# Optimization experiments

Hardware: AMD Instinct MI355X
Metric: run time of the kernel (lower is better)

Reference implementation:

```python
import jax, jax.numpy as jnp
import numpy as np


def setup_inputs() -> dict:
    key = jax.random.key(0)
    ks = jax.random.split(key, 9)
    U, H, R, N = 32, 5120, 160, 16
    return {
        "x": jax.random.normal(ks[0], (U, H), jnp.float32),
        "W_delta": jax.random.normal(ks[1], (H, R), jnp.float32) * 0.02,
        "W_dt": jax.random.normal(ks[2], (R, H), jnp.float32) * 0.02,
        "b_dt": jax.random.normal(ks[3], (H,), jnp.float32) * 0.02,
        "W_B": jax.random.normal(ks[4], (H, N), jnp.float32) * 0.02,
        "W_C": jax.random.normal(ks[5], (H, N), jnp.float32) * 0.02,
        "A_log": jax.random.uniform(ks[6], (H, N), jnp.float32),
        "D": jax.random.normal(ks[7], (H,), jnp.float32),
        "h": jax.random.normal(ks[8], (U, H, N), jnp.float32),
    }


def reference(x, W_delta, W_dt, b_dt, W_B, W_C, A_log, D, h):
    # x: (U,H) single-token decode for U users; h: (U,H,N) recurrent state.
    # delta: low-rank projection then dt_proj, softplus
    dt = jax.nn.softplus((x @ W_delta) @ W_dt + b_dt)          # (U,H)
    A = -jnp.exp(A_log)                                        # (H,N)
    abar = jnp.exp(dt[:, :, None] * A[None, :, :])             # (U,H,N)
    B = x @ W_B                                                # (U,N)
    C = x @ W_C                                                # (U,N)
    # state update: h' = abar*h + (dt*B)*x
    h_new = abar * h + dt[:, :, None] * B[:, None, :] * x[:, :, None]  # (U,H,N)
    # output mix: y = C . h' + D*x
    y = jnp.einsum("uhn,un->uh", h_new, C) + x * D[None, :]    # (U,H)
    return y
```

## Files before the change

kernel.cpp:

```cpp
#include <hip/hip_runtime.h>
#include <math.h>

#define UU 32
#define HH 5120
#define RR 160
#define NN 16


__device__ __forceinline__ unsigned short f2bf(float f) {
    unsigned int u = __float_as_uint(f);
    u += 0x7fffu + ((u >> 16) & 1u);
    return (unsigned short)(u >> 16);
}
__device__ __forceinline__ float blo(unsigned int v) { return __uint_as_float(v << 16); }
__device__ __forceinline__ float bhi(unsigned int v) { return __uint_as_float(v & 0xffff0000u); }

__global__ __launch_bounds__(256) void proj_kernel(
    const float* __restrict__ x, const float* __restrict__ Wd,
    const float* __restrict__ WB, const float* __restrict__ WC,
    float* __restrict__ ws)
{
    __shared__ float xs[32 * 36];
    __shared__ float wt[32 * 160];

    const int b = blockIdx.x;
    const int t = threadIdx.x;

    if (b < 80) {
        const int u0 = (t >> 5) * 4;
        const int r0 = (t & 31) * 5;
        float acc[4][5];
        #pragma unroll
        for (int i = 0; i < 4; i++)
            #pragma unroll
            for (int j = 0; j < 5; j++) acc[i][j] = 0.f;

        #pragma unroll
        for (int c = 0; c < 2; c++) {
            const int k0 = b * 64 + c * 32;
            if (c) __syncthreads();
            #pragma unroll
            for (int i = 0; i < 4; i++) {
                int idx = t + i * 256;
                int u = idx >> 5, kk = idx & 31;
                xs[kk * 36 + u] = x[u * HH + k0 + kk];
            }
            #pragma unroll
            for (int i = 0; i < 5; i++) {
                int idx4 = t + i * 256;
                *(float4*)&wt[idx4 * 4] = ((const float4*)(Wd + k0 * RR))[idx4];
            }
            __syncthreads();

            #pragma unroll
            for (int kk = 0; kk < 32; kk++) {
                float4 xv = *(const float4*)&xs[kk * 36 + u0];
                float wv[5];
                #pragma unroll
                for (int j = 0; j < 5; j++) wv[j] = wt[kk * 160 + r0 + j];
                const float xi[4] = {xv.x, xv.y, xv.z, xv.w};
                #pragma unroll
                for (int i = 0; i < 4; i++)
                    #pragma unroll
                    for (int j = 0; j < 5; j++) acc[i][j] += xi[i] * wv[j];
            }
        }
        #pragma unroll
        for (int i = 0; i < 4; i++)
            #pragma unroll
            for (int j = 0; j < 5; j++)
                atomicAdd(&ws[(u0 + i) * 160 + (r0 + j)], acc[i][j]);
    } else {
        const int bc = b - 80;
        const int k0 = bc * 160;
        const int n = t & 15;
        const int uu = t >> 4;
        const float* xa = x + uu * HH;
        const float* xb = x + (uu + 16) * HH;
        float aB0 = 0.f, aB1 = 0.f, aC0 = 0.f, aC1 = 0.f;
        #pragma unroll 8
        for (int k = k0; k < k0 + 160; k++) {
            float wb = WB[k * NN + n];
            float wc = WC[k * NN + n];
            float va = xa[k], vb = xb[k];
            aB0 += va * wb; aB1 += vb * wb;
            aC0 += va * wc; aC1 += vb * wc;
        }
        atomicAdd(&ws[5120 + uu * 16 + n], aB0);
        atomicAdd(&ws[5120 + (uu + 16) * 16 + n], aB1);
        atomicAdd(&ws[5632 + uu * 16 + n], aC0);
        atomicAdd(&ws[5632 + (uu + 16) * 16 + n], aC1);
    }
}

__device__ __forceinline__ float softplusf(float v) {
    return (v > 20.f) ? v : log1pf(expf(v));
}

__global__ __launch_bounds__(256) void ssm_kernel(
    const float* __restrict__ x, const float* __restrict__ Wdt,
    const float* __restrict__ bdt, const float* __restrict__ Alog,
    const float* __restrict__ Dv, const float* __restrict__ hstate,
    const float* __restrict__ ws, float* __restrict__ y)
{
    __shared__ unsigned short tmp_b[32 * 168];
    __shared__ unsigned short wsl_b[16 * 168];
    __shared__ float Bl[32 * 20];
    __shared__ float Cl[32 * 20];
    __shared__ float an_l[16 * 20];
    __shared__ float xl[32 * 17];
    __shared__ float bdtl[16];
    __shared__ float Dl[16];

    const int t  = threadIdx.x;
    const int h0 = blockIdx.x * 16;
    const int u  = t >> 3;
    const int q  = t & 7;

    const float* hb0 = hstate + (size_t)(u * HH + h0 + q) * 16;
    const float* hb1 = hstate + (size_t)(u * HH + h0 + q + 8) * 16;
    float4 hv0[4], hv1[4];
    #pragma unroll
    for (int k = 0; k < 4; k++) { hv0[k] = ((const float4*)hb0)[k]; hv1[k] = ((const float4*)hb1)[k]; }

    #pragma unroll
    for (int i = 0; i < 5; i++) {
        int idx4 = t + i * 256;
        int uu = idx4 / 40, r4 = idx4 % 40;
        float4 v = ((const float4*)ws)[idx4];
        unsigned int p0 = (unsigned int)f2bf(v.x) | ((unsigned int)f2bf(v.y) << 16);
        unsigned int p1 = (unsigned int)f2bf(v.z) | ((unsigned int)f2bf(v.w) << 16);
        *(uint2*)&tmp_b[uu * 168 + r4 * 4] = make_uint2(p0, p1);
    }
    #pragma unroll
    for (int i = 0; i < 10; i++) {
        int idx = t + i * 256;
        int r = idx >> 4, hh = idx & 15;
        wsl_b[hh * 168 + r] = f2bf(Wdt[r * HH + h0 + hh]);
    }
    #pragma unroll
    for (int i = 0; i < 2; i++) {
        int idx = t + i * 256;
        int uu = idx >> 4, n = idx & 15;
        Bl[uu * 20 + n] = ws[5120 + idx];
        Cl[uu * 20 + n] = ws[5632 + idx];
        xl[uu * 17 + n] = x[uu * HH + h0 + n];
    }
    {
        int hh = t >> 4, n = t & 15;
        an_l[hh * 20 + n] = -expf(Alog[(h0 + hh) * 16 + n]);
    }
    if (t < 16) { bdtl[t] = bdt[h0 + t]; Dl[t] = Dv[h0 + t]; }
    __syncthreads();

    const uint4* ta = (const uint4*)&tmp_b[u * 168];
    const uint4* w0p = (const uint4*)&wsl_b[q * 168];
    const uint4* w1p = (const uint4*)&wsl_b[(q + 8) * 168];
    float a0e = 0.f, a0o = 0.f, a1e = 0.f, a1o = 0.f;
    #pragma unroll
    for (int c = 0; c < 20; c++) {
        uint4 av = ta[c];
        uint4 w0 = w0p[c];
        uint4 w1 = w1p[c];
        #define MAC(X) \
            a0e += blo(av.X) * blo(w0.X); a0o += bhi(av.X) * bhi(w0.X); \
            a1e += blo(av.X) * blo(w1.X); a1o += bhi(av.X) * bhi(w1.X);
        MAC(x) MAC(y) MAC(z) MAC(w)
        #undef MAC
    }
    const float dt0 = softplusf(bdtl[q]     + (a0e + a0o));
    const float dt1 = softplusf(bdtl[q + 8] + (a1e + a1o));

    #pragma unroll
    for (int j = 0; j < 2; j++) {
        const int hh = q + j * 8;
        const float dt = j ? dt1 : dt0;
        const float xv = xl[u * 17 + hh];
        const float K  = dt * xv;
        float yv = xv * Dl[hh];
        const float4* hv = j ? hv1 : hv0;
        #pragma unroll
        for (int qq = 0; qq < 4; qq++) {
            float4 h4 = hv[qq];
            float4 bq = *(const float4*)&Bl[u * 20 + qq * 4];
            float4 cq = *(const float4*)&Cl[u * 20 + qq * 4];
            float4 av = *(const float4*)&an_l[hh * 20 + qq * 4];
            yv += (expf(dt * av.x) * h4.x + K * bq.x) * cq.x;
            yv += (expf(dt * av.y) * h4.y + K * bq.y) * cq.y;
            yv += (expf(dt * av.z) * h4.z + K * bq.z) * cq.z;
            yv += (expf(dt * av.w) * h4.w + K * bq.w) * cq.w;
        }
        y[u * HH + h0 + hh] = yv;
    }
}

extern "C" void kernel_launch(void* const* d_in, const int* in_sizes, int n_in,
                              void* d_out, int out_size, void* d_ws, size_t ws_size,
                              hipStream_t stream) {
    const float* x    = (const float*)d_in[0];
    const float* Wd   = (const float*)d_in[1];
    const float* Wdt  = (const float*)d_in[2];
    const float* bdt  = (const float*)d_in[3];
    const float* WB   = (const float*)d_in[4];
    const float* WC   = (const float*)d_in[5];
    const float* Alog = (const float*)d_in[6];
    const float* Dv   = (const float*)d_in[7];
    const float* hst  = (const float*)d_in[8];
    float* y  = (float*)d_out;
    float* ws = (float*)d_ws;

    proj_kernel<<<112, 256, 0, stream>>>(x, Wd, WB, WC, ws);
    ssm_kernel<<<320, 256, 0, stream>>>(x, Wdt, bdt, Alog, Dv, hst, ws, y);
}
```

Before: 113.8 us.

## Replace atomic accumulation with split-K partial buffers reduced in consumer kernel

The projection kernel now writes per-split partial sums of the low-rank delta and B/C projections into separate workspace slices instead of using atomicAdd on shared locations. The SSM kernel sums the 16 slices while staging data into shared memory. The SSM kernel also moves to 512 threads with one channel per thread. This removes atomic contention and any need for a zeroed workspace, at the cost of every SSM block redundantly re-reading and reducing the partial buffers.

```diff
diff --git a/kernel.cpp b/kernel.cpp
--- a/kernel.cpp
+++ b/kernel.cpp
@@ -6,6 +6,10 @@
 #define RR 160
 #define NN 16
 
+
+#define TMP_WS 0
+#define BP_WS  81920
+#define CP_WS  90112
 
 __device__ __forceinline__ unsigned short f2bf(float f) {
     unsigned int u = __float_as_uint(f);
@@ -21,23 +25,21 @@
     float* __restrict__ ws)
 {
     __shared__ float xs[32 * 36];
-    __shared__ float wt[32 * 160];
+    __shared__ float wt[32 * 32];
 
     const int b = blockIdx.x;
     const int t = threadIdx.x;
 
     if (b < 80) {
+        const int s  = b & 15;
+        const int rt = b >> 4;
+        const int r0 = rt * 32;
         const int u0 = (t >> 5) * 4;
-        const int r0 = (t & 31) * 5;
-        float acc[4][5];
-        #pragma unroll
-        for (int i = 0; i < 4; i++)
-            #pragma unroll
-            for (int j = 0; j < 5; j++) acc[i][j] = 0.f;
-
-        #pragma unroll
-        for (int c = 0; c < 2; c++) {
-            const int k0 = b * 64 + c * 32;
+        const int r  = t & 31;
+        float acc[4] = {0.f, 0.f, 0.f, 0.f};
+
+        for (int c = 0; c < 10; c++) {
+            const int k0 = s * 320 + c * 32;
             if (c) __syncthreads();
             #pragma unroll
             for (int i = 0; i < 4; i++) {
@@ -45,51 +47,49 @@
                 int u = idx >> 5, kk = idx & 31;
                 xs[kk * 36 + u] = x[u * HH + k0 + kk];
             }
-            #pragma unroll
-            for (int i = 0; i < 5; i++) {
-                int idx4 = t + i * 256;
-                *(float4*)&wt[idx4 * 4] = ((const float4*)(Wd + k0 * RR))[idx4];
+            {
+                int kk = t >> 3, c4 = t & 7;
+                *(float4*)&wt[kk * 32 + c4 * 4] =
+                    *(const float4*)(Wd + (size_t)(k0 + kk) * RR + r0 + c4 * 4);
             }
             __syncthreads();
 
             #pragma unroll
             for (int kk = 0; kk < 32; kk++) {
                 float4 xv = *(const float4*)&xs[kk * 36 + u0];
-                float wv[5];
-                #pragma unroll
-                for (int j = 0; j < 5; j++) wv[j] = wt[kk * 160 + r0 + j];
-                const float xi[4] = {xv.x, xv.y, xv.z, xv.w};
-                #pragma unroll
-                for (int i = 0; i < 4; i++)
-                    #pragma unroll
-                    for (int j = 0; j < 5; j++) acc[i][j] += xi[i] * wv[j];
+                float wv = wt[kk * 32 + r];
+                acc[0] += xv.x * wv; acc[1] += xv.y * wv;
+                acc[2] += xv.z * wv; acc[3] += xv.w * wv;
             }
         }
         #pragma unroll
         for (int i = 0; i < 4; i++)
-            #pragma unroll
-            for (int j = 0; j < 5; j++)
-                atomicAdd(&ws[(u0 + i) * 160 + (r0 + j)], acc[i][j]);
+            ws[TMP_WS + s * 5120 + (u0 + i) * 160 + r0 + r] = acc[i];
     } else {
-        const int bc = b - 80;
-        const int k0 = bc * 160;
-        const int n = t & 15;
+        const int sb = b - 80;
+        const int k0 = sb * 320;
+        const int n  = t & 15;
         const int uu = t >> 4;
-        const float* xa = x + uu * HH;
-        const float* xb = x + (uu + 16) * HH;
+        const float* xa = x + uu * HH + k0;
+        const float* xb = x + (uu + 16) * HH + k0;
         float aB0 = 0.f, aB1 = 0.f, aC0 = 0.f, aC1 = 0.f;
-        #pragma unroll 8
-        for (int k = k0; k < k0 + 160; k++) {
-            float wb = WB[k * NN + n];
-            float wc = WC[k * NN + n];
-            float va = xa[k], vb = xb[k];
-            aB0 += va * wb; aB1 += vb * wb;
-            aC0 += va * wc; aC1 += vb * wc;
-        }
-        atomicAdd(&ws[5120 + uu * 16 + n], aB0);
-        atomicAdd(&ws[5120 + (uu + 16) * 16 + n], aB1);
-        atomicAdd(&ws[5632 + uu * 16 + n], aC0);
-        atomicAdd(&ws[5632 + (uu + 16) * 16 + n], aC1);
+        #pragma unroll 2
+        for (int k4 = 0; k4 < 80; k4++) {
+            float4 va = *(const float4*)(xa + k4 * 4);
+            float4 vb = *(const float4*)(xb + k4 * 4);
+            const int kb = (k0 + k4 * 4) * NN + n;
+            #define STEP(D, CMP) { \
+                float wb = WB[kb + (D) * NN]; \
+                float wc = WC[kb + (D) * NN]; \
+                aB0 += va.CMP * wb; aB1 += vb.CMP * wb; \
+                aC0 += va.CMP * wc; aC1 += vb.CMP * wc; }
+            STEP(0, x) STEP(1, y) STEP(2, z) STEP(3, w)
+            #undef STEP
+        }
+        ws[BP_WS + sb * 512 + uu * 16 + n]        = aB0;
+        ws[BP_WS + sb * 512 + (uu + 16) * 16 + n] = aB1;
+        ws[CP_WS + sb * 512 + uu * 16 + n]        = aC0;
+        ws[CP_WS + sb * 512 + (uu + 16) * 16 + n] = aC1;
     }
 }
 
@@ -97,7 +97,7 @@
     return (v > 20.f) ? v : log1pf(expf(v));
 }
 
-__global__ __launch_bounds__(256) void ssm_kernel(
+__global__ __launch_bounds__(512) void ssm_kernel(
     const float* __restrict__ x, const float* __restrict__ Wdt,
     const float* __restrict__ bdt, const float* __restrict__ Alog,
     const float* __restrict__ Dv, const float* __restrict__ hstate,
@@ -114,39 +114,49 @@
 
     const int t  = threadIdx.x;
     const int h0 = blockIdx.x * 16;
-    const int u  = t >> 3;
-    const int q  = t & 7;
-
-    const float* hb0 = hstate + (size_t)(u * HH + h0 + q) * 16;
-    const float* hb1 = hstate + (size_t)(u * HH + h0 + q + 8) * 16;
-    float4 hv0[4], hv1[4];
-    #pragma unroll
-    for (int k = 0; k < 4; k++) { hv0[k] = ((const float4*)hb0)[k]; hv1[k] = ((const float4*)hb1)[k]; }
-
+    const int u  = t >> 4;
+    const int q  = t & 15;
+
+    const float* hb = hstate + (size_t)(u * HH + h0 + q) * 16;
+    float4 hv[4];
+    #pragma unroll
+    for (int k = 0; k < 4; k++) hv[k] = ((const float4*)hb)[k];
+
+    #pragma unroll
+    for (int i = 0; i < 3; i++) {
+        int idx4 = t + i * 512;
+        if (idx4 < 1280) {
+            float sx = 0.f, sy = 0.f, sz = 0.f, sw = 0.f;
+            #pragma unroll
+            for (int s = 0; s < 16; s++) {
+                float4 v = ((const float4*)(ws + TMP_WS + s * 5120))[idx4];
+                sx += v.x; sy += v.y; sz += v.z; sw += v.w;
+            }
+            int uu = idx4 / 40, r4 = idx4 % 40;
+            unsigned int p0 = (unsigned int)f2bf(sx) | ((unsigned int)f2bf(sy) << 16);
+            unsigned int p1 = (unsigned int)f2bf(sz) | ((unsigned int)f2bf(sw) << 16);
+            *(uint2*)&tmp_b[uu * 168 + r4 * 4] = make_uint2(p0, p1);
+        }
+    }
     #pragma unroll
     for (int i = 0; i < 5; i++) {
-        int idx4 = t + i * 256;
-        int uu = idx4 / 40, r4 = idx4 % 40;
-        float4 v = ((const float4*)ws)[idx4];
-        unsigned int p0 = (unsigned int)f2bf(v.x) | ((unsigned int)f2bf(v.y) << 16);
-        unsigned int p1 = (unsigned int)f2bf(v.z) | ((unsigned int)f2bf(v.w) << 16);
-        *(uint2*)&tmp_b[uu * 168 + r4 * 4] = make_uint2(p0, p1);
-    }
-    #pragma unroll
-    for (int i = 0; i < 10; i++) {
-        int idx = t + i * 256;
+        int idx = t + i * 512;
         int r = idx >> 4, hh = idx & 15;
         wsl_b[hh * 168 + r] = f2bf(Wdt[r * HH + h0 + hh]);
     }
-    #pragma unroll
-    for (int i = 0; i < 2; i++) {
-        int idx = t + i * 256;
-        int uu = idx >> 4, n = idx & 15;
-        Bl[uu * 20 + n] = ws[5120 + idx];
-        Cl[uu * 20 + n] = ws[5632 + idx];
+    {
+        int uu = t >> 4, n = t & 15;
+        float sb = 0.f, sc = 0.f;
+        #pragma unroll
+        for (int s = 0; s < 16; s++) {
+            sb += ws[BP_WS + s * 512 + t];
+            sc += ws[CP_WS + s * 512 + t];
+        }
+        Bl[uu * 20 + n] = sb;
+        Cl[uu * 20 + n] = sc;
         xl[uu * 17 + n] = x[uu * HH + h0 + n];
     }
-    {
+    if (t < 256) {
         int hh = t >> 4, n = t & 15;
         an_l[hh * 20 + n] = -expf(Alog[(h0 + hh) * 16 + n]);
     }
@@ -154,44 +164,34 @@
     __syncthreads();
 
     const uint4* ta = (const uint4*)&tmp_b[u * 168];
-    const uint4* w0p = (const uint4*)&wsl_b[q * 168];
-    const uint4* w1p = (const uint4*)&wsl_b[(q + 8) * 168];
-    float a0e = 0.f, a0o = 0.f, a1e = 0.f, a1o = 0.f;
+    const uint4* wp = (const uint4*)&wsl_b[q * 168];
+    float ae = 0.f, ao = 0.f;
     #pragma unroll
     for (int c = 0; c < 20; c++) {
         uint4 av = ta[c];
-        uint4 w0 = w0p[c];
-        uint4 w1 = w1p[c];
+        uint4 wv = wp[c];
         #define MAC(X) \
-            a0e += blo(av.X) * blo(w0.X); a0o += bhi(av.X) * bhi(w0.X); \
-            a1e += blo(av.X) * blo(w1.X); a1o += bhi(av.X) * bhi(w1.X);
+            ae += blo(av.X) * blo(wv.X); ao += bhi(av.X) * bhi(wv.X);
         MAC(x) MAC(y) MAC(z) MAC(w)
         #undef MAC
     }
-    const float dt0 = softplusf(bdtl[q]     + (a0e + a0o));
-    const float dt1 = softplusf(bdtl[q + 8] + (a1e + a1o));
-
-    #pragma unroll
-    for (int j = 0; j < 2; j++) {
-        const int hh = q + j * 8;
-        const float dt = j ? dt1 : dt0;
-        const float xv = xl[u * 17 + hh];
-        const float K  = dt * xv;
-        float yv = xv * Dl[hh];
-        const float4* hv = j ? hv1 : hv0;
-        #pragma unroll
-        for (int qq = 0; qq < 4; qq++) {
-            float4 h4 = hv[qq];
-            float4 bq = *(const float4*)&Bl[u * 20 + qq * 4];
-            float4 cq = *(const float4*)&Cl[u * 20 + qq * 4];
-            float4 av = *(const float4*)&an_l[hh * 20 + qq * 4];
-            yv += (expf(dt * av.x) * h4.x + K * bq.x) * cq.x;
-            yv += (expf(dt * av.y) * h4.y + K * bq.y) * cq.y;
-            yv += (expf(dt * av.z) * h4.z + K * bq.z) * cq.z;
-            yv += (expf(dt * av.w) * h4.w + K * bq.w) * cq.w;
-        }
-        y[u * HH + h0 + hh] = yv;
-    }
+    const float dt = softplusf(bdtl[q] + (ae + ao));
+
+    const float xv = xl[u * 17 + q];
+    const float K  = dt * xv;
+    float yv = xv * Dl[q];
+    #pragma unroll
+    for (int qq = 0; qq < 4; qq++) {
+        float4 h4 = hv[qq];
+        float4 b4 = *(const float4*)&Bl[u * 20 + qq * 4];
+        float4 c4 = *(const float4*)&Cl[u * 20 + qq * 4];
+        float4 a4 = *(const float4*)&an_l[q * 20 + qq * 4];
+        yv += (expf(dt * a4.x) * h4.x + K * b4.x) * c4.x;
+        yv += (expf(dt * a4.y) * h4.y + K * b4.y) * c4.y;
+        yv += (expf(dt * a4.z) * h4.z + K * b4.z) * c4.z;
+        yv += (expf(dt * a4.w) * h4.w + K * b4.w) * c4.w;
+    }
+    y[u * HH + h0 + q] = yv;
 }
 
 extern "C" void kernel_launch(void* const* d_in, const int* in_sizes, int n_in,
@@ -209,6 +209,6 @@
     float* y  = (float*)d_out;
     float* ws = (float*)d_ws;
 
-    proj_kernel<<<112, 256, 0, stream>>>(x, Wd, WB, WC, ws);
-    ssm_kernel<<<320, 256, 0, stream>>>(x, Wdt, bdt, Alog, Dv, hst, ws, y);
-}
+    proj_kernel<<<96, 256, 0, stream>>>(x, Wd, WB, WC, ws);
+    ssm_kernel<<<320, 512, 0, stream>>>(x, Wdt, bdt, Alog, Dv, hst, ws, y);
+}
```

After: 108.6 us. 1.05x faster.
